# Performance work log

Measured on AMD Instinct MI355X. Metric: run time of the kernel, lower is better.

## Reference

```python
import jax, jax.numpy as jnp
import numpy as np

N = 50000      # nodes
E = 800000     # edges (avg degree 16)
IN, HID, OUT = 128, 256, 64
G = 500        # graphs in the batch (100 nodes each)
NEG_SLOPE = 0.01
EPS = 1e-12


def setup_inputs() -> dict:
    key = jax.random.key(0)
    ks = jax.random.split(key, 9)
    x = jax.random.normal(ks[0], (N, IN), jnp.float32)
    edge_index = jax.random.randint(ks[1], (2, E), 0, N, dtype=jnp.int32)
    # sorted segment ids with every graph present (100 nodes per graph)
    batch = jnp.repeat(jnp.arange(G, dtype=jnp.int32), N // G)
    def lin(k, fan_in, fan_out):
        s = 1.0 / np.sqrt(fan_in)
        kw, kb = jax.random.split(k)
        W = jax.random.uniform(kw, (fan_in, fan_out), jnp.float32, -s, s)
        b = jax.random.uniform(kb, (fan_out,), jnp.float32, -s, s)
        return W, b
    W1, b1 = lin(ks[2], IN, HID)
    W2, b2 = lin(ks[3], HID, HID)
    W3, b3 = lin(ks[4], HID, OUT)
    return {"x": x, "edge_index": edge_index, "batch": batch,
            "W1": W1, "b1": b1, "W2": W2, "b2": b2, "W3": W3, "b3": b3}


def _sage_conv(x, edge_index, W, b):
    # SAGEConv(aggr='add', root_weight=False, normalize=True):
    # gather source features, scatter-add to targets, linear, L2 normalize.
    src, dst = edge_index[0], edge_index[1]
    agg = jax.ops.segment_sum(x[src], dst, num_segments=x.shape[0])  # [N, d_in]
    out = agg @ W + b                                                 # [N, d_out]
    nrm = jnp.linalg.norm(out, axis=-1, keepdims=True)
    return out / jnp.maximum(nrm, EPS)


def reference(x, edge_index, batch, W1, b1, W2, b2, W3, b3):
    h = _sage_conv(x, edge_index, W1, b1)
    h = jax.nn.leaky_relu(h, NEG_SLOPE)          # dropout p=0 -> identity
    h = _sage_conv(h, edge_index, W2, b2)
    h = jax.nn.leaky_relu(h, NEG_SLOPE)
    h = _sage_conv(h, edge_index, W3, b3)
    # get_zero_nodes: first node of each graph (batch sorted, all G present)
    mask = jnp.concatenate([jnp.ones((1,), bool), batch[1:] != batch[:-1]])
    first_idx = jnp.nonzero(mask, size=G)[0]
    return h[first_idx]                          # [G, OUT]
```

## Files before the change

### kernel.cpp

```cpp
#include <hip/hip_runtime.h>

#define N_NODES 50000
#define E_EDGES 800000
#define IN_DIM  128
#define HID_DIM 256
#define OUT_DIM 64
#define G_GRAPHS 500
#define CAP 64
#define NBINS 196
#define BINCAP 5120

typedef __attribute__((ext_vector_type(8))) short short8;
typedef __attribute__((ext_vector_type(4))) float float4v;

__device__ __forceinline__ float bf2f(unsigned short u) {
  union { unsigned int i; float f; } c; c.i = ((unsigned int)u) << 16; return c.f;
}
__device__ __forceinline__ unsigned short f2bf(float f) {
  union { float f; unsigned int i; } c; c.f = f;
  unsigned int x = c.i;
  x += 0x7FFFu + ((x >> 16) & 1u);
  return (unsigned short)(x >> 16);
}
__device__ __forceinline__ unsigned int fbits(float f) {
  union { float f; unsigned int i; } c; c.f = f; return c.i;
}
__device__ __forceinline__ float bits2f(unsigned int u) {
  union { unsigned int i; float f; } c; c.i = u; return c.f;
}


__global__ __launch_bounds__(256) void prep1(
    const int* __restrict__ src, const int* __restrict__ dst,
    const int* __restrict__ batch,
    const float* __restrict__ x,
    const float* __restrict__ W1, const float* __restrict__ W2,
    unsigned int* __restrict__ binbuf, int* __restrict__ bin_next,
    unsigned char* __restrict__ is_first,
    unsigned short* __restrict__ xb,
    unsigned short* __restrict__ W1t, unsigned short* __restrict__ W2t) {
  const int b = blockIdx.x, tid = threadIdx.x;
  if (b < 200) {
    __shared__ int cnt[NBINS];
    __shared__ int gbase[NBINS];
    for (int i = tid; i < NBINS; i += 256) cnt[i] = 0;
    __syncthreads();
    const int base = b * 4096;
    unsigned int pk[16]; int bp[16];
#pragma unroll
    for (int u = 0; u < 16; ++u) {
      const int e = base + u * 256 + tid;
      bp[u] = -1;
      if (e < E_EDGES) {
        const int d = dst[e];
        const int s = src[e];
        const int bin = d >> 8;
        const int pos = atomicAdd(&cnt[bin], 1);
        pk[u] = ((unsigned int)(d & 255) << 16) | (unsigned int)s;
        bp[u] = (bin << 16) | pos;
      }
    }
    __syncthreads();
    for (int i = tid; i < NBINS; i += 256)
      gbase[i] = atomicAdd(&bin_next[i], cnt[i]);
    __syncthreads();
#pragma unroll
    for (int u = 0; u < 16; ++u) {
      if (bp[u] >= 0) {
        const int bin = bp[u] >> 16, pos = bp[u] & 0xFFFF;
        const int idx = gbase[bin] + pos;
        if (idx < BINCAP) binbuf[bin * BINCAP + idx] = pk[u];
      }
    }
  } else if (b < 6450) {
    const int t = (b - 200) * 256 + tid;
    const int i = t * 4;
    const float4 v = *(const float4*)(x + i);
    ushort4 u;
    u.x = f2bf(v.x); u.y = f2bf(v.y); u.z = f2bf(v.z); u.w = f2bf(v.w);
    *(ushort4*)(xb + i) = u;
    if (t < N_NODES) {
      is_first[t] = (t == 0 || batch[t] != batch[t - 1]) ? 1 : 0;
    }
  } else {
    const int t = (b - 6450) * 256 + tid;
    if (t < 8192) {
      const int n = t >> 5, k0 = (t & 31) * 4;
      ushort4 o;
      o.x = f2bf(W1[(k0 + 0) * 256 + n]);
      o.y = f2bf(W1[(k0 + 1) * 256 + n]);
      o.z = f2bf(W1[(k0 + 2) * 256 + n]);
      o.w = f2bf(W1[(k0 + 3) * 256 + n]);
      *(ushort4*)&W1t[n * 128 + k0] = o;
    } else {
      const int v2 = t - 8192;
      const int n = v2 >> 6, k0 = (v2 & 63) * 4;
      ushort4 o;
      o.x = f2bf(W2[(k0 + 0) * 256 + n]);
      o.y = f2bf(W2[(k0 + 1) * 256 + n]);
      o.z = f2bf(W2[(k0 + 2) * 256 + n]);
      o.w = f2bf(W2[(k0 + 3) * 256 + n]);
      *(ushort4*)&W2t[n * 256 + k0] = o;
    }
  }
}


__global__ __launch_bounds__(512) void prep2(
    const unsigned int* __restrict__ binbuf, const int* __restrict__ bin_next,
    const int* __restrict__ batch, const unsigned char* __restrict__ is_first,
    int* __restrict__ deg, unsigned short* __restrict__ srcs,
    unsigned short* __restrict__ list2, int* __restrict__ l2cnt) {
  __shared__ unsigned short img[256 * CAP];
  __shared__ int cnt[256];
  const int tid = threadIdx.x;
  const int bin = blockIdx.x;
  if (tid < 256) cnt[tid] = 0;
  __syncthreads();
  const int total = min(bin_next[bin], BINCAP);
  const unsigned int* bb = binbuf + bin * BINCAP;
  for (int i = tid; i < total; i += 512) {
    const unsigned int pk = bb[i];
    const int nl = pk >> 16;
    const int pos = atomicAdd(&cnt[nl], 1);
    if (pos < CAP) img[(nl << 6) + pos] = (unsigned short)(pk & 0xFFFFu);
  }
  __syncthreads();
  const int node0 = bin << 8;
  const int nend = min(N_NODES, node0 + 256);
  if (tid < 256 && node0 + tid < nend) {
    const int c = cnt[tid];
    deg[node0 + tid] = c;
    if (is_first[node0 + tid]) {
      const int g = batch[node0 + tid];
      l2cnt[g] = min(c, CAP);
      unsigned int* d = (unsigned int*)(list2 + g * 64);
      const unsigned int* s = (const unsigned int*)(img + (tid << 6));
      for (int q = 0; q < 32; ++q) d[q] = s[q];
    }
  }
  const int nwords = (nend - node0) * 32;
  unsigned int* dstw = (unsigned int*)(srcs + ((size_t)node0 << 6));
  const unsigned int* srcw = (const unsigned int*)img;
  for (int i = tid; i < nwords; i += 512) dstw[i] = srcw[i];
}


template<int K, int MODE>
__global__ __launch_bounds__(512, 8) void fused_layer(
    const unsigned short* __restrict__ H,
    const int* __restrict__ deg, const unsigned short* __restrict__ srcs,
    const unsigned short* __restrict__ Wt,
    const float* __restrict__ bias,
    unsigned short* __restrict__ Hout,
    const unsigned short* __restrict__ list2,
    const int* __restrict__ l2cnt,
    float* __restrict__ agg_part)
{
  constexpr int M = 256;
  constexpr int TN = 16;
  constexpr int VPT = K / 64;
  constexpr int LDK = K + 8;
  __shared__ unsigned short a_hi[TN][LDK];
  __shared__ unsigned short a_lo[TN][LDK];
  __shared__ float ssq_tot[TN];
  __shared__ float vld_s[TN];
  __shared__ int nid_s[TN];
  const int tid = threadIdx.x;
  const int lane = tid & 63;
  const int wv = tid >> 6;
  const int graph = blockIdx.x % G_GRAPHS;
  const int p = blockIdx.x / G_GRAPHS;

  if (tid < TN) {
    if constexpr (MODE == 1) {
      const int slot = p * 16 + tid;
      const bool vld = slot < l2cnt[graph];
      nid_s[tid] = vld ? (int)list2[graph * 64 + slot] : 0;
      vld_s[tid] = vld ? 1.f : 0.f;
    } else {
      nid_s[tid] = blockIdx.x * TN + tid;
      vld_s[tid] = 1.f;
    }
    ssq_tot[tid] = 0.f;
  }
  __syncthreads();

  const unsigned short* hb = H + lane * VPT;
  const int node0 = __builtin_amdgcn_readfirstlane(nid_s[2 * wv]);
  const int node1 = __builtin_amdgcn_readfirstlane(nid_s[2 * wv + 1]);
  int cnt0 = __builtin_amdgcn_readfirstlane(min(deg[node0], CAP));
  int cnt1 = __builtin_amdgcn_readfirstlane(min(deg[node1], CAP));
  if constexpr (MODE == 1) {
    if (vld_s[2 * wv] == 0.f) cnt0 = 0;
    if (vld_s[2 * wv + 1] == 0.f) cnt1 = 0;
  }
  int idx0 = 0, idx1 = 0;
  if (lane < cnt0) idx0 = srcs[(node0 << 6) + lane];
  if (lane < cnt1) idx1 = srcs[(node1 << 6) + lane];

  float acc0[VPT], acc1[VPT];
#pragma unroll
  for (int q = 0; q < VPT; ++q) { acc0[q] = 0.f; acc1[q] = 0.f; }
  int j0 = 0, j1 = 0;

  if constexpr (VPT == 2) {
    while (j0 + 16 <= cnt0 && j1 + 16 <= cnt1) {
      int s0[16], s1[16];
#pragma unroll
      for (int u = 0; u < 16; ++u) {
        s0[u] = __builtin_amdgcn_readlane(idx0, j0 + u);
        s1[u] = __builtin_amdgcn_readlane(idx1, j1 + u);
      }
      ushort2 r0[16], r1[16];
#pragma unroll
      for (int u = 0; u < 16; ++u) r0[u] = *(const ushort2*)(hb + s0[u] * K);
#pragma unroll
      for (int u = 0; u < 16; ++u) r1[u] = *(const ushort2*)(hb + s1[u] * K);
#pragma unroll
      for (int u = 0; u < 16; ++u) {
        acc0[0] += bf2f(r0[u].x); acc0[1] += bf2f(r0[u].y);
        acc1[0] += bf2f(r1[u].x); acc1[1] += bf2f(r1[u].y);
      }
      j0 += 16; j1 += 16;
    }
  }

#pragma unroll
  for (int i = 0; i < 2; ++i) {
    const int nn = 2 * wv + i;
    const int cnt = i ? cnt1 : cnt0;
    const int idx = i ? idx1 : idx0;
    float (&acc)[VPT] = i ? acc1 : acc0;
    int j = i ? j1 : j0;

    for (; j + 16 <= cnt; j += 16) {
      int s[16];
#pragma unroll
      for (int u = 0; u < 16; ++u) s[u] = __builtin_amdgcn_readlane(idx, j + u);
      if constexpr (VPT == 4) {
        ushort4 r[16];
#pragma unroll
        for (int u = 0; u < 16; ++u) r[u] = *(const ushort4*)(hb + s[u] * K);
#pragma unroll
        for (int u = 0; u < 16; ++u) {
          acc[0] += bf2f(r[u].x); acc[1] += bf2f(r[u].y);
          acc[2] += bf2f(r[u].z); acc[3] += bf2f(r[u].w);
        }
      } else {
        ushort2 r[16];
#pragma unroll
        for (int u = 0; u < 16; ++u) r[u] = *(const ushort2*)(hb + s[u] * K);
#pragma unroll
        for (int u = 0; u < 16; ++u) {
          acc[0] += bf2f(r[u].x); acc[1] += bf2f(r[u].y);
        }
      }
    }
    for (; j < cnt; j += 8) {
      int s[8]; float w[8];
#pragma unroll
      for (int u = 0; u < 8; ++u) {
        const int q = j + u;
        const int qm = (q < cnt) ? q : (cnt - 1);
        s[u] = __builtin_amdgcn_readlane(idx, qm);
        w[u] = (q < cnt) ? 1.f : 0.f;
      }
      if constexpr (VPT == 4) {
        ushort4 r[8];
#pragma unroll
        for (int u = 0; u < 8; ++u) r[u] = *(const ushort4*)(hb + s[u] * K);
#pragma unroll
        for (int u = 0; u < 8; ++u) {
          acc[0] = fmaf(w[u], bf2f(r[u].x), acc[0]);
          acc[1] = fmaf(w[u], bf2f(r[u].y), acc[1]);
          acc[2] = fmaf(w[u], bf2f(r[u].z), acc[2]);
          acc[3] = fmaf(w[u], bf2f(r[u].w), acc[3]);
        }
      } else {
        ushort2 r[8];
#pragma unroll
        for (int u = 0; u < 8; ++u) r[u] = *(const ushort2*)(hb + s[u] * K);
#pragma unroll
        for (int u = 0; u < 8; ++u) {
          acc[0] = fmaf(w[u], bf2f(r[u].x), acc[0]);
          acc[1] = fmaf(w[u], bf2f(r[u].y), acc[1]);
        }
      }
    }

    unsigned short h[VPT], l[VPT];
#pragma unroll
    for (int jj = 0; jj < VPT; ++jj) {
      const unsigned int u = fbits(acc[jj]);
      h[jj] = (unsigned short)(u >> 16);
      const float res = acc[jj] - bits2f(u & 0xFFFF0000u);
      l[jj] = (unsigned short)(fbits(res) >> 16);
    }
    if constexpr (VPT == 4) {
      *(ushort4*)&a_hi[nn][lane * 4] = make_ushort4(h[0], h[1], h[2], h[3]);
      *(ushort4*)&a_lo[nn][lane * 4] = make_ushort4(l[0], l[1], l[2], l[3]);
    } else {
      *(ushort2*)&a_hi[nn][lane * 2] = make_ushort2(h[0], h[1]);
      *(ushort2*)&a_lo[nn][lane * 2] = make_ushort2(l[0], l[1]);
    }
  }
  __syncthreads();

  const int g = lane >> 4;
  const int lc = lane & 15;
  float4v dacc0 = (float4v){0.f, 0.f, 0.f, 0.f};
  float4v dacc1 = (float4v){0.f, 0.f, 0.f, 0.f};
  const unsigned short* W0 = Wt + (size_t)(wv * 16 + lc) * K + g * 8;
  const unsigned short* W1r = Wt + (size_t)((wv + 8) * 16 + lc) * K + g * 8;
#pragma unroll
  for (int ks = 0; ks < K / 32; ++ks) {
    const short8 ah = *(const short8*)&a_hi[lc][ks * 32 + g * 8];
    const short8 al = *(const short8*)&a_lo[lc][ks * 32 + g * 8];
    const short8 b0 = *(const short8*)(W0 + ks * 32);
    const short8 b1 = *(const short8*)(W1r + ks * 32);
    dacc0 = __builtin_amdgcn_mfma_f32_16x16x32_bf16(ah, b0, dacc0, 0, 0, 0);
    dacc0 = __builtin_amdgcn_mfma_f32_16x16x32_bf16(al, b0, dacc0, 0, 0, 0);
    dacc1 = __builtin_amdgcn_mfma_f32_16x16x32_bf16(ah, b1, dacc1, 0, 0, 0);
    dacc1 = __builtin_amdgcn_mfma_f32_16x16x32_bf16(al, b1, dacc1, 0, 0, 0);
  }

  const float bn0 = bias[wv * 16 + lc];
  const float bn1 = bias[(wv + 8) * 16 + lc];
  float4v o0 = dacc0 + bn0;
  float4v o1 = dacc1 + bn1;
  float sq[4];
#pragma unroll
  for (int r = 0; r < 4; ++r) sq[r] = o0[r] * o0[r] + o1[r] * o1[r];
#pragma unroll
  for (int off = 1; off < 16; off <<= 1) {
#pragma unroll
    for (int r = 0; r < 4; ++r) sq[r] += __shfl_xor(sq[r], off);
  }
  if (lc == 0) {
#pragma unroll
    for (int r = 0; r < 4; ++r) atomicAdd(&ssq_tot[g * 4 + r], sq[r]);
  }
  __syncthreads();

  if constexpr (MODE == 0) {
#pragma unroll
    for (int r = 0; r < 4; ++r) {
      const float inv = 1.f / fmaxf(sqrtf(ssq_tot[g * 4 + r]), 1e-12f);
      float v0 = o0[r] * inv;
      float v1 = o1[r] * inv;
      v0 = (v0 >= 0.f) ? v0 : 0.01f * v0;
      v1 = (v1 >= 0.f) ? v1 : 0.01f * v1;
      const int nd = nid_s[g * 4 + r];
      Hout[(size_t)nd * M + wv * 16 + lc] = f2bf(v0);
      Hout[(size_t)nd * M + (wv + 8) * 16 + lc] = f2bf(v1);
    }
  } else {
    float s0 = 0.f, s1 = 0.f;
#pragma unroll
    for (int r = 0; r < 4; ++r) {
      const float inv = 1.f / fmaxf(sqrtf(ssq_tot[g * 4 + r]), 1e-12f);
      float v0 = o0[r] * inv;
      float v1 = o1[r] * inv;
      v0 = (v0 >= 0.f) ? v0 : 0.01f * v0;
      v1 = (v1 >= 0.f) ? v1 : 0.01f * v1;
      const float w = vld_s[g * 4 + r];
      s0 += w * v0; s1 += w * v1;
    }
    s0 += __shfl_xor(s0, 16); s0 += __shfl_xor(s0, 32);
    s1 += __shfl_xor(s1, 16); s1 += __shfl_xor(s1, 32);
    if (lane < 16) {
      float* pp = agg_part + ((size_t)(graph * 4 + p) << 8);
      pp[wv * 16 + lane] = s0;
      pp[128 + wv * 16 + lane] = s1;
    }
  }
}


__global__ __launch_bounds__(64) void layer3_kernel(
    const float* __restrict__ agg_part,
    const float* __restrict__ W,
    const float* __restrict__ bias,
    float* __restrict__ out)
{
  __shared__ float a_s[HID_DIM];
  const int g = blockIdx.x;
  const int lane = threadIdx.x;
  const float* pp = agg_part + ((size_t)g << 10);
#pragma unroll
  for (int c = 0; c < 4; ++c) {
    const int idx = c * 64 + lane;
    a_s[idx] = pp[idx] + pp[256 + idx] + pp[512 + idx] + pp[768 + idx];
  }
  __syncthreads();
  float o = bias[lane];
#pragma unroll 8
  for (int k = 0; k < HID_DIM; ++k) o += a_s[k] * W[k * OUT_DIM + lane];
  float ss = o * o;
#pragma unroll
  for (int off = 32; off > 0; off >>= 1) ss += __shfl_xor(ss, off);
  const float inv = 1.f / fmaxf(sqrtf(ss), 1e-12f);
  out[(size_t)g * OUT_DIM + lane] = o * inv;
}


extern "C" void kernel_launch(void* const* d_in, const int* in_sizes, int n_in,
                              void* d_out, int out_size, void* d_ws, size_t ws_size,
                              hipStream_t stream) {
  (void)in_sizes; (void)n_in; (void)out_size; (void)ws_size;
  const float* x   = (const float*)d_in[0];
  const int* ei    = (const int*)d_in[1];
  const int* batch = (const int*)d_in[2];
  const float* W1  = (const float*)d_in[3];
  const float* b1  = (const float*)d_in[4];
  const float* W2  = (const float*)d_in[5];
  const float* b2  = (const float*)d_in[6];
  const float* W3  = (const float*)d_in[7];
  const float* b3  = (const float*)d_in[8];
  const int* src = ei;
  const int* dst = ei + E_EDGES;

  char* ws = (char*)d_ws;
  size_t off = 0;
  auto alloc = [&](size_t bytes) {
    void* p = ws + off;
    off = (off + bytes + 255) & ~(size_t)255;
    return p;
  };
  int* bin_next = (int*)alloc((size_t)NBINS * 4);
  const size_t zero_len = off;

  int* deg    = (int*)alloc((size_t)N_NODES * 4);
  unsigned short* srcs = (unsigned short*)alloc((size_t)N_NODES * CAP * 2);
  unsigned char* is_first = (unsigned char*)alloc((size_t)N_NODES);
  unsigned short* list2 = (unsigned short*)alloc((size_t)G_GRAPHS * CAP * 2);
  int* l2cnt  = (int*)alloc((size_t)G_GRAPHS * 4);
  unsigned int* binbuf = (unsigned int*)alloc((size_t)NBINS * BINCAP * 4);
  float* agg_part = (float*)alloc((size_t)G_GRAPHS * 4 * 256 * 4);
  unsigned short* W1t = (unsigned short*)alloc((size_t)256 * 128 * 2);
  unsigned short* W2t = (unsigned short*)alloc((size_t)256 * 256 * 2);
  unsigned short* xb = (unsigned short*)alloc((size_t)N_NODES * IN_DIM * 2);
  unsigned short* h1 = (unsigned short*)alloc((size_t)N_NODES * HID_DIM * 2);

  hipMemsetAsync(bin_next, 0, zero_len, stream);

  prep1<<<6546, 256, 0, stream>>>(src, dst, batch, x, W1, W2,
                                  binbuf, bin_next, is_first, xb, W1t, W2t);
  prep2<<<NBINS, 512, 0, stream>>>(binbuf, bin_next, batch, is_first,
                                   deg, srcs, list2, l2cnt);

  fused_layer<IN_DIM, 0><<<N_NODES / 16, 512, 0, stream>>>(
      xb, deg, srcs, W1t, b1, h1, nullptr, nullptr, nullptr);
  fused_layer<HID_DIM, 1><<<G_GRAPHS * 4, 512, 0, stream>>>(
      h1, deg, srcs, W2t, b2, nullptr, list2, l2cnt, agg_part);
  layer3_kernel<<<G_GRAPHS, 64, 0, stream>>>(agg_part, W3, b3, (float*)d_out);
}
```

Measured before the change: 205.0 us.

## Fuse all stages into one persistent cooperative kernel with grid syncs

Result: slower. 537.1 us (+162.0%).

```diff
diff --git a/kernel.cpp b/kernel.cpp
--- a/kernel.cpp
+++ b/kernel.cpp
@@ -1,4 +1,7 @@
 #include <hip/hip_runtime.h>
+#include <hip/hip_cooperative_groups.h>
+
+namespace cg = cooperative_groups;
 
 #define N_NODES 50000
 #define E_EDGES 800000
@@ -7,8 +10,15 @@
 #define OUT_DIM 64
 #define G_GRAPHS 500
 #define CAP 64
-#define NBINS 196
-#define BINCAP 5120
+#define NBINS 391
+#define BINCAP 2816
+#define NSORT 200
+#define NXCV 3125
+#define NWCV 48
+#define NL1 (N_NODES / 16)
+#define NL2 (G_GRAPHS * 4)
+#define NL3 63
+#define SMEM_BYTES 17536
 
 typedef __attribute__((ext_vector_type(8))) short short8;
 typedef __attribute__((ext_vector_type(4))) float float4v;
@@ -30,92 +40,87 @@
 }
 
 
-__global__ __launch_bounds__(256) void prep1(
+__device__ __forceinline__ void xconv_vb(int v, int tid,
+    const float* __restrict__ x, const int* __restrict__ batch,
+    unsigned char* __restrict__ is_first, unsigned short* __restrict__ xb) {
+  const int t = v * 512 + tid;
+  const int i = t * 4;
+  const float4 vv = *(const float4*)(x + i);
+  ushort4 u;
+  u.x = f2bf(vv.x); u.y = f2bf(vv.y); u.z = f2bf(vv.z); u.w = f2bf(vv.w);
+  *(ushort4*)(xb + i) = u;
+  if (t < N_NODES) is_first[t] = (t == 0 || batch[t] != batch[t - 1]) ? 1 : 0;
+}
+
+__device__ __forceinline__ void wconv_vb(int v, int tid,
+    const float* __restrict__ W1, const float* __restrict__ W2,
+    unsigned short* __restrict__ W1t, unsigned short* __restrict__ W2t) {
+  const int t = v * 512 + tid;
+  if (t < 8192) {
+    const int n = t >> 5, k0 = (t & 31) * 4;
+    ushort4 o;
+    o.x = f2bf(W1[(k0 + 0) * 256 + n]);
+    o.y = f2bf(W1[(k0 + 1) * 256 + n]);
+    o.z = f2bf(W1[(k0 + 2) * 256 + n]);
+    o.w = f2bf(W1[(k0 + 3) * 256 + n]);
+    *(ushort4*)&W1t[n * 128 + k0] = o;
+  } else {
+    const int v2 = t - 8192;
+    const int n = v2 >> 6, k0 = (v2 & 63) * 4;
+    ushort4 o;
+    o.x = f2bf(W2[(k0 + 0) * 256 + n]);
+    o.y = f2bf(W2[(k0 + 1) * 256 + n]);
+    o.z = f2bf(W2[(k0 + 2) * 256 + n]);
+    o.w = f2bf(W2[(k0 + 3) * 256 + n]);
+    *(ushort4*)&W2t[n * 256 + k0] = o;
+  }
+}
+
+__device__ void sort_vb(int sb, int tid, void* smemraw,
     const int* __restrict__ src, const int* __restrict__ dst,
-    const int* __restrict__ batch,
-    const float* __restrict__ x,
-    const float* __restrict__ W1, const float* __restrict__ W2,
-    unsigned int* __restrict__ binbuf, int* __restrict__ bin_next,
-    unsigned char* __restrict__ is_first,
-    unsigned short* __restrict__ xb,
-    unsigned short* __restrict__ W1t, unsigned short* __restrict__ W2t) {
-  const int b = blockIdx.x, tid = threadIdx.x;
-  if (b < 200) {
-    __shared__ int cnt[NBINS];
-    __shared__ int gbase[NBINS];
-    for (int i = tid; i < NBINS; i += 256) cnt[i] = 0;
-    __syncthreads();
-    const int base = b * 4096;
-    unsigned int pk[16]; int bp[16];
-#pragma unroll
-    for (int u = 0; u < 16; ++u) {
-      const int e = base + u * 256 + tid;
-      bp[u] = -1;
-      if (e < E_EDGES) {
-        const int d = dst[e];
-        const int s = src[e];
-        const int bin = d >> 8;
-        const int pos = atomicAdd(&cnt[bin], 1);
-        pk[u] = ((unsigned int)(d & 255) << 16) | (unsigned int)s;
-        bp[u] = (bin << 16) | pos;
-      }
-    }
-    __syncthreads();
-    for (int i = tid; i < NBINS; i += 256)
-      gbase[i] = atomicAdd(&bin_next[i], cnt[i]);
-    __syncthreads();
-#pragma unroll
-    for (int u = 0; u < 16; ++u) {
-      if (bp[u] >= 0) {
-        const int bin = bp[u] >> 16, pos = bp[u] & 0xFFFF;
-        const int idx = gbase[bin] + pos;
-        if (idx < BINCAP) binbuf[bin * BINCAP + idx] = pk[u];
-      }
-    }
-  } else if (b < 6450) {
-    const int t = (b - 200) * 256 + tid;
-    const int i = t * 4;
-    const float4 v = *(const float4*)(x + i);
-    ushort4 u;
-    u.x = f2bf(v.x); u.y = f2bf(v.y); u.z = f2bf(v.z); u.w = f2bf(v.w);
-    *(ushort4*)(xb + i) = u;
-    if (t < N_NODES) {
-      is_first[t] = (t == 0 || batch[t] != batch[t - 1]) ? 1 : 0;
-    }
-  } else {
-    const int t = (b - 6450) * 256 + tid;
-    if (t < 8192) {
-      const int n = t >> 5, k0 = (t & 31) * 4;
-      ushort4 o;
-      o.x = f2bf(W1[(k0 + 0) * 256 + n]);
-      o.y = f2bf(W1[(k0 + 1) * 256 + n]);
-      o.z = f2bf(W1[(k0 + 2) * 256 + n]);
-      o.w = f2bf(W1[(k0 + 3) * 256 + n]);
-      *(ushort4*)&W1t[n * 128 + k0] = o;
-    } else {
-      const int v2 = t - 8192;
-      const int n = v2 >> 6, k0 = (v2 & 63) * 4;
-      ushort4 o;
-      o.x = f2bf(W2[(k0 + 0) * 256 + n]);
-      o.y = f2bf(W2[(k0 + 1) * 256 + n]);
-      o.z = f2bf(W2[(k0 + 2) * 256 + n]);
-      o.w = f2bf(W2[(k0 + 3) * 256 + n]);
-      *(ushort4*)&W2t[n * 256 + k0] = o;
-    }
-  }
-}
-
-
-__global__ __launch_bounds__(512) void prep2(
+    unsigned int* __restrict__ binbuf, int* __restrict__ bin_next) {
+  int* cnt = (int*)smemraw;
+  int* gbase = cnt + NBINS;
+  for (int i = tid; i < NBINS; i += 512) cnt[i] = 0;
+  __syncthreads();
+  const int base = sb * 4096;
+  unsigned int pk[8]; int bp[8];
+#pragma unroll
+  for (int u = 0; u < 8; ++u) {
+    const int e = base + u * 512 + tid;
+    bp[u] = -1;
+    if (e < E_EDGES) {
+      const int d = dst[e];
+      const int s = src[e];
+      const int bin = d >> 7;
+      const int pos = atomicAdd(&cnt[bin], 1);
+      pk[u] = ((unsigned int)(d & 127) << 16) | (unsigned int)s;
+      bp[u] = (bin << 16) | pos;
+    }
+  }
+  __syncthreads();
+  for (int i = tid; i < NBINS; i += 512)
+    gbase[i] = atomicAdd(&bin_next[i], cnt[i]);
+  __syncthreads();
+#pragma unroll
+  for (int u = 0; u < 8; ++u) {
+    if (bp[u] >= 0) {
+      const int bin = bp[u] >> 16, pos = bp[u] & 0xFFFF;
+      const int idx = gbase[bin] + pos;
+      if (idx < BINCAP) binbuf[bin * BINCAP + idx] = pk[u];
+    }
+  }
+  __syncthreads();
+}
+
+__device__ void bucket_vb(int bin, int tid, void* smemraw,
     const unsigned int* __restrict__ binbuf, const int* __restrict__ bin_next,
     const int* __restrict__ batch, const unsigned char* __restrict__ is_first,
     int* __restrict__ deg, unsigned short* __restrict__ srcs,
     unsigned short* __restrict__ list2, int* __restrict__ l2cnt) {
-  __shared__ unsigned short img[256 * CAP];
-  __shared__ int cnt[256];
-  const int tid = threadIdx.x;
-  const int bin = blockIdx.x;
-  if (tid < 256) cnt[tid] = 0;
+  unsigned short* img = (unsigned short*)smemraw;
+  int* cnt = (int*)(img + 128 * CAP);
+  if (tid < 128) cnt[tid] = 0;
   __syncthreads();
   const int total = min(bin_next[bin], BINCAP);
   const unsigned int* bb = binbuf + bin * BINCAP;
@@ -126,51 +131,47 @@
     if (pos < CAP) img[(nl << 6) + pos] = (unsigned short)(pk & 0xFFFFu);
   }
   __syncthreads();
-  const int node0 = bin << 8;
-  const int nend = min(N_NODES, node0 + 256);
-  if (tid < 256 && node0 + tid < nend) {
+  const int node0 = bin << 7;
+  const int nend = min(N_NODES, node0 + 128);
+  if (tid < 128 && node0 + tid < nend) {
     const int c = cnt[tid];
     deg[node0 + tid] = c;
     if (is_first[node0 + tid]) {
       const int g = batch[node0 + tid];
       l2cnt[g] = min(c, CAP);
-      unsigned int* d = (unsigned int*)(list2 + g * 64);
-      const unsigned int* s = (const unsigned int*)(img + (tid << 6));
-      for (int q = 0; q < 32; ++q) d[q] = s[q];
+      unsigned int* dW = (unsigned int*)(list2 + g * 64);
+      const unsigned int* sW = (const unsigned int*)(img + (tid << 6));
+      for (int q = 0; q < 32; ++q) dW[q] = sW[q];
     }
   }
   const int nwords = (nend - node0) * 32;
   unsigned int* dstw = (unsigned int*)(srcs + ((size_t)node0 << 6));
   const unsigned int* srcw = (const unsigned int*)img;
   for (int i = tid; i < nwords; i += 512) dstw[i] = srcw[i];
-}
-
+  __syncthreads();
+}
 
 template<int K, int MODE>
-__global__ __launch_bounds__(512, 8) void fused_layer(
+__device__ void fused_vb(int vb, int tid, void* smemraw,
     const unsigned short* __restrict__ H,
     const int* __restrict__ deg, const unsigned short* __restrict__ srcs,
-    const unsigned short* __restrict__ Wt,
-    const float* __restrict__ bias,
+    const unsigned short* __restrict__ Wt, const float* __restrict__ bias,
     unsigned short* __restrict__ Hout,
-    const unsigned short* __restrict__ list2,
-    const int* __restrict__ l2cnt,
-    float* __restrict__ agg_part)
-{
+    const unsigned short* __restrict__ list2, const int* __restrict__ l2cnt,
+    float* __restrict__ agg_part) {
   constexpr int M = 256;
   constexpr int TN = 16;
   constexpr int VPT = K / 64;
   constexpr int LDK = K + 8;
-  __shared__ unsigned short a_hi[TN][LDK];
-  __shared__ unsigned short a_lo[TN][LDK];
-  __shared__ float ssq_tot[TN];
-  __shared__ float vld_s[TN];
-  __shared__ int nid_s[TN];
-  const int tid = threadIdx.x;
+  unsigned short (*a_hi)[LDK] = (unsigned short(*)[LDK])smemraw;
+  unsigned short (*a_lo)[LDK] = (unsigned short(*)[LDK])((char*)smemraw + TN * LDK * 2);
+  float* ssq_tot = (float*)((char*)smemraw + TN * LDK * 4);
+  float* vld_s = ssq_tot + TN;
+  int* nid_s = (int*)(vld_s + TN);
   const int lane = tid & 63;
   const int wv = tid >> 6;
-  const int graph = blockIdx.x % G_GRAPHS;
-  const int p = blockIdx.x / G_GRAPHS;
+  const int graph = vb % G_GRAPHS;
+  const int p = vb / G_GRAPHS;
 
   if (tid < TN) {
     if constexpr (MODE == 1) {
@@ -179,7 +180,7 @@
       nid_s[tid] = vld ? (int)list2[graph * 64 + slot] : 0;
       vld_s[tid] = vld ? 1.f : 0.f;
     } else {
-      nid_s[tid] = blockIdx.x * TN + tid;
+      nid_s[tid] = vb * TN + tid;
       vld_s[tid] = 1.f;
     }
     ssq_tot[tid] = 0.f;
@@ -375,33 +376,100 @@
       pp[128 + wv * 16 + lane] = s1;
     }
   }
-}
-
-
-__global__ __launch_bounds__(64) void layer3_kernel(
-    const float* __restrict__ agg_part,
-    const float* __restrict__ W,
-    const float* __restrict__ bias,
-    float* __restrict__ out)
-{
-  __shared__ float a_s[HID_DIM];
-  const int g = blockIdx.x;
-  const int lane = threadIdx.x;
-  const float* pp = agg_part + ((size_t)g << 10);
-#pragma unroll
-  for (int c = 0; c < 4; ++c) {
-    const int idx = c * 64 + lane;
-    a_s[idx] = pp[idx] + pp[256 + idx] + pp[512 + idx] + pp[768 + idx];
-  }
-  __syncthreads();
-  float o = bias[lane];
+  __syncthreads();
+}
+
+__device__ void l3_vb(int v, int tid, void* smemraw,
+    const float* __restrict__ agg_part, const float* __restrict__ W,
+    const float* __restrict__ bias, float* __restrict__ out) {
+  const int wv = tid >> 6, lane = tid & 63;
+  const int g = v * 8 + wv;
+  float* a_s = (float*)smemraw + wv * 256;
+  if (g < G_GRAPHS) {
+    const float* pp = agg_part + ((size_t)g << 10);
+#pragma unroll
+    for (int c = 0; c < 4; ++c) {
+      const int idx = c * 64 + lane;
+      a_s[idx] = pp[idx] + pp[256 + idx] + pp[512 + idx] + pp[768 + idx];
+    }
+  }
+  __syncthreads();
+  if (g < G_GRAPHS) {
+    float o = bias[lane];
 #pragma unroll 8
-  for (int k = 0; k < HID_DIM; ++k) o += a_s[k] * W[k * OUT_DIM + lane];
-  float ss = o * o;
-#pragma unroll
-  for (int off = 32; off > 0; off >>= 1) ss += __shfl_xor(ss, off);
-  const float inv = 1.f / fmaxf(sqrtf(ss), 1e-12f);
-  out[(size_t)g * OUT_DIM + lane] = o * inv;
+    for (int k = 0; k < HID_DIM; ++k) o += a_s[k] * W[k * OUT_DIM + lane];
+    float ss = o * o;
+#pragma unroll
+    for (int off = 32; off > 0; off >>= 1) ss += __shfl_xor(ss, off);
+    const float inv = 1.f / fmaxf(sqrtf(ss), 1e-12f);
+    out[(size_t)g * OUT_DIM + lane] = o * inv;
+  }
+  __syncthreads();
+}
+
+__global__ __launch_bounds__(512, 8) void mega(
+    const int* src, const int* dst, const int* batch, const float* x,
+    const float* W1, const float* W2, const float* b1, const float* b2,
+    const float* W3, const float* b3,
+    unsigned int* binbuf, int* bin_next, unsigned char* is_first,
+    unsigned short* xb, unsigned short* W1t, unsigned short* W2t,
+    int* deg, unsigned short* srcs, unsigned short* list2, int* l2cnt,
+    unsigned short* h1, float* agg_part, float* outp) {
+  __shared__ __align__(16) char smem[SMEM_BYTES];
+  cg::grid_group grid = cg::this_grid();
+  const int tid = threadIdx.x;
+  const int nb = gridDim.x;
+  for (int v = blockIdx.x; v < NXCV + NWCV + NSORT; v += nb) {
+    if (v < NXCV) xconv_vb(v, tid, x, batch, is_first, xb);
+    else if (v < NXCV + NWCV) wconv_vb(v - NXCV, tid, W1, W2, W1t, W2t);
+    else sort_vb(v - NXCV - NWCV, tid, smem, src, dst, binbuf, bin_next);
+  }
+  grid.sync();
+  for (int v = blockIdx.x; v < NBINS; v += nb)
+    bucket_vb(v, tid, smem, binbuf, bin_next, batch, is_first, deg, srcs, list2, l2cnt);
+  grid.sync();
+  for (int v = blockIdx.x; v < NL1; v += nb)
+    fused_vb<IN_DIM, 0>(v, tid, smem, xb, deg, srcs, W1t, b1, h1, nullptr, nullptr, nullptr);
+  grid.sync();
+  for (int v = blockIdx.x; v < NL2; v += nb)
+    fused_vb<HID_DIM, 1>(v, tid, smem, h1, deg, srcs, W2t, b2, nullptr, list2, l2cnt, agg_part);
+  grid.sync();
+  for (int v = blockIdx.x; v < NL3; v += nb)
+    l3_vb(v, tid, smem, agg_part, W3, b3, outp);
+}
+
+__global__ __launch_bounds__(512, 8) void wrapA1(
+    const int* src, const int* dst, const int* batch, const float* x,
+    const float* W1, const float* W2,
+    unsigned int* binbuf, int* bin_next, unsigned char* is_first,
+    unsigned short* xb, unsigned short* W1t, unsigned short* W2t) {
+  __shared__ __align__(16) char smem[SMEM_BYTES];
+  const int v = blockIdx.x, tid = threadIdx.x;
+  if (v < NXCV) xconv_vb(v, tid, x, batch, is_first, xb);
+  else if (v < NXCV + NWCV) wconv_vb(v - NXCV, tid, W1, W2, W1t, W2t);
+  else sort_vb(v - NXCV - NWCV, tid, smem, src, dst, binbuf, bin_next);
+}
+__global__ __launch_bounds__(512, 8) void wrapA2(
+    const unsigned int* binbuf, const int* bin_next, const int* batch,
+    const unsigned char* is_first, int* deg, unsigned short* srcs,
+    unsigned short* list2, int* l2cnt) {
+  __shared__ __align__(16) char smem[SMEM_BYTES];
+  bucket_vb(blockIdx.x, threadIdx.x, smem, binbuf, bin_next, batch, is_first,
+            deg, srcs, list2, l2cnt);
+}
+template<int K, int MODE>
+__global__ __launch_bounds__(512, 8) void wrapF(
+    const unsigned short* H, const int* deg, const unsigned short* srcs,
+    const unsigned short* Wt, const float* bias, unsigned short* Hout,
+    const unsigned short* list2, const int* l2cnt, float* agg_part) {
+  __shared__ __align__(16) char smem[SMEM_BYTES];
+  fused_vb<K, MODE>(blockIdx.x, threadIdx.x, smem, H, deg, srcs, Wt, bias,
+                    Hout, list2, l2cnt, agg_part);
+}
+__global__ __launch_bounds__(512, 8) void wrapD(
+    const float* agg_part, const float* W, const float* bias, float* out) {
+  __shared__ __align__(16) char smem[SMEM_BYTES];
+  l3_vb(blockIdx.x, threadIdx.x, smem, agg_part, W, bias, out);
 }
 
 
@@ -420,6 +488,7 @@
   const float* b3  = (const float*)d_in[8];
   const int* src = ei;
   const int* dst = ei + E_EDGES;
+  float* outp = (float*)d_out;
 
   char* ws = (char*)d_ws;
   size_t off = 0;
@@ -430,7 +499,6 @@
   };
   int* bin_next = (int*)alloc((size_t)NBINS * 4);
   const size_t zero_len = off;
-
   int* deg    = (int*)alloc((size_t)N_NODES * 4);
   unsigned short* srcs = (unsigned short*)alloc((size_t)N_NODES * CAP * 2);
   unsigned char* is_first = (unsigned char*)alloc((size_t)N_NODES);
@@ -445,14 +513,32 @@
 
   hipMemsetAsync(bin_next, 0, zero_len, stream);
 
-  prep1<<<6546, 256, 0, stream>>>(src, dst, batch, x, W1, W2,
-                                  binbuf, bin_next, is_first, xb, W1t, W2t);
-  prep2<<<NBINS, 512, 0, stream>>>(binbuf, bin_next, batch, is_first,
-                                   deg, srcs, list2, l2cnt);
-
-  fused_layer<IN_DIM, 0><<<N_NODES / 16, 512, 0, stream>>>(
-      xb, deg, srcs, W1t, b1, h1, nullptr, nullptr, nullptr);
-  fused_layer<HID_DIM, 1><<<G_GRAPHS * 4, 512, 0, stream>>>(
-      h1, deg, srcs, W2t, b2, nullptr, list2, l2cnt, agg_part);
-  layer3_kernel<<<G_GRAPHS, 64, 0, stream>>>(agg_part, W3, b3, (float*)d_out);
-}
+  int occ = 0;
+  hipOccupancyMaxActiveBlocksPerMultiprocessor(&occ, mega, 512, 0);
+  int grid = occ * 256;
+  if (grid > 1024) grid = 1024;
+  bool coop = (grid >= 256);
+  if (coop) {
+    void* args[] = {
+      (void*)&src, (void*)&dst, (void*)&batch, (void*)&x,
+      (void*)&W1, (void*)&W2, (void*)&b1, (void*)&b2, (void*)&W3, (void*)&b3,
+      (void*)&binbuf, (void*)&bin_next, (void*)&is_first,
+      (void*)&xb, (void*)&W1t, (void*)&W2t,
+      (void*)&deg, (void*)&srcs, (void*)&list2, (void*)&l2cnt,
+      (void*)&h1, (void*)&agg_part, (void*)&outp };
+    hipError_t e = hipLaunchCooperativeKernel(mega, dim3(grid), dim3(512),
+                                              args, 0u, stream);
+    coop = (e == hipSuccess);
+  }
+  if (!coop) {
+    wrapA1<<<NXCV + NWCV + NSORT, 512, 0, stream>>>(
+        src, dst, batch, x, W1, W2, binbuf, bin_next, is_first, xb, W1t, W2t);
+    wrapA2<<<NBINS, 512, 0, stream>>>(
+        binbuf, bin_next, batch, is_first, deg, srcs, list2, l2cnt);
+    wrapF<IN_DIM, 0><<<NL1, 512, 0, stream>>>(
+        xb, deg, srcs, W1t, b1, h1, nullptr, nullptr, nullptr);
+    wrapF<HID_DIM, 1><<<NL2, 512, 0, stream>>>(
+        h1, deg, srcs, W2t, b2, nullptr, list2, l2cnt, agg_part);
+    wrapD<<<NL3, 512, 0, stream>>>(agg_part, W3, b3, outp);
+  }
+}
```

## Split wave into half-waves per node with wider gathers; skip empty layer-2 blocks

Applied to the files above, without the earlier changes.

New measurement: 201.6 us. Within noise of the previous version (-1.7%).

```diff
diff --git a/kernel.cpp b/kernel.cpp
--- a/kernel.cpp
+++ b/kernel.cpp
@@ -12,6 +12,8 @@
 
 typedef __attribute__((ext_vector_type(8))) short short8;
 typedef __attribute__((ext_vector_type(4))) float float4v;
+typedef __attribute__((ext_vector_type(4))) unsigned short u16x4;
+typedef __attribute__((ext_vector_type(8))) unsigned short u16x8;
 
 __device__ __forceinline__ float bf2f(unsigned short u) {
   union { unsigned int i; float f; } c; c.i = ((unsigned int)u) << 16; return c.f;
@@ -159,7 +161,8 @@
 {
   constexpr int M = 256;
   constexpr int TN = 16;
-  constexpr int VPT = K / 64;
+  constexpr int CH = K / 32;
+  constexpr int DEPTH = (CH == 4) ? 16 : 8;
   constexpr int LDK = K + 8;
   __shared__ unsigned short a_hi[TN][LDK];
   __shared__ unsigned short a_lo[TN][LDK];
@@ -172,6 +175,10 @@
   const int graph = blockIdx.x % G_GRAPHS;
   const int p = blockIdx.x / G_GRAPHS;
 
+  if constexpr (MODE == 1) {
+    if (p * 16 >= l2cnt[graph]) return;
+  }
+
   if (tid < TN) {
     if constexpr (MODE == 1) {
       const int slot = p * 16 + tid;
@@ -186,7 +193,8 @@
   }
   __syncthreads();
 
-  const unsigned short* hb = H + lane * VPT;
+  const int half = lane >> 5;
+  const int li = lane & 31;
   const int node0 = __builtin_amdgcn_readfirstlane(nid_s[2 * wv]);
   const int node1 = __builtin_amdgcn_readfirstlane(nid_s[2 * wv + 1]);
   int cnt0 = __builtin_amdgcn_readfirstlane(min(deg[node0], CAP));
@@ -198,111 +206,75 @@
   int idx0 = 0, idx1 = 0;
   if (lane < cnt0) idx0 = srcs[(node0 << 6) + lane];
   if (lane < cnt1) idx1 = srcs[(node1 << 6) + lane];
-
-  float acc0[VPT], acc1[VPT];
-#pragma unroll
-  for (int q = 0; q < VPT; ++q) { acc0[q] = 0.f; acc1[q] = 0.f; }
-  int j0 = 0, j1 = 0;
-
-  if constexpr (VPT == 2) {
-    while (j0 + 16 <= cnt0 && j1 + 16 <= cnt1) {
-      int s0[16], s1[16];
-#pragma unroll
-      for (int u = 0; u < 16; ++u) {
-        s0[u] = __builtin_amdgcn_readlane(idx0, j0 + u);
-        s1[u] = __builtin_amdgcn_readlane(idx1, j1 + u);
-      }
-      ushort2 r0[16], r1[16];
-#pragma unroll
-      for (int u = 0; u < 16; ++u) r0[u] = *(const ushort2*)(hb + s0[u] * K);
-#pragma unroll
-      for (int u = 0; u < 16; ++u) r1[u] = *(const ushort2*)(hb + s1[u] * K);
-#pragma unroll
-      for (int u = 0; u < 16; ++u) {
-        acc0[0] += bf2f(r0[u].x); acc0[1] += bf2f(r0[u].y);
-        acc1[0] += bf2f(r1[u].x); acc1[1] += bf2f(r1[u].y);
-      }
-      j0 += 16; j1 += 16;
-    }
-  }
-
-#pragma unroll
-  for (int i = 0; i < 2; ++i) {
-    const int nn = 2 * wv + i;
-    const int cnt = i ? cnt1 : cnt0;
-    const int idx = i ? idx1 : idx0;
-    float (&acc)[VPT] = i ? acc1 : acc0;
-    int j = i ? j1 : j0;
-
-    for (; j + 16 <= cnt; j += 16) {
-      int s[16];
-#pragma unroll
-      for (int u = 0; u < 16; ++u) s[u] = __builtin_amdgcn_readlane(idx, j + u);
-      if constexpr (VPT == 4) {
-        ushort4 r[16];
-#pragma unroll
-        for (int u = 0; u < 16; ++u) r[u] = *(const ushort4*)(hb + s[u] * K);
-#pragma unroll
-        for (int u = 0; u < 16; ++u) {
-          acc[0] += bf2f(r[u].x); acc[1] += bf2f(r[u].y);
-          acc[2] += bf2f(r[u].z); acc[3] += bf2f(r[u].w);
-        }
-      } else {
-        ushort2 r[16];
-#pragma unroll
-        for (int u = 0; u < 16; ++u) r[u] = *(const ushort2*)(hb + s[u] * K);
-#pragma unroll
-        for (int u = 0; u < 16; ++u) {
-          acc[0] += bf2f(r[u].x); acc[1] += bf2f(r[u].y);
-        }
-      }
-    }
-    for (; j < cnt; j += 8) {
-      int s[8]; float w[8];
-#pragma unroll
-      for (int u = 0; u < 8; ++u) {
-        const int q = j + u;
-        const int qm = (q < cnt) ? q : (cnt - 1);
-        s[u] = __builtin_amdgcn_readlane(idx, qm);
-        w[u] = (q < cnt) ? 1.f : 0.f;
-      }
-      if constexpr (VPT == 4) {
-        ushort4 r[8];
-#pragma unroll
-        for (int u = 0; u < 8; ++u) r[u] = *(const ushort4*)(hb + s[u] * K);
-#pragma unroll
-        for (int u = 0; u < 8; ++u) {
-          acc[0] = fmaf(w[u], bf2f(r[u].x), acc[0]);
-          acc[1] = fmaf(w[u], bf2f(r[u].y), acc[1]);
-          acc[2] = fmaf(w[u], bf2f(r[u].z), acc[2]);
-          acc[3] = fmaf(w[u], bf2f(r[u].w), acc[3]);
-        }
-      } else {
-        ushort2 r[8];
-#pragma unroll
-        for (int u = 0; u < 8; ++u) r[u] = *(const ushort2*)(hb + s[u] * K);
-#pragma unroll
-        for (int u = 0; u < 8; ++u) {
-          acc[0] = fmaf(w[u], bf2f(r[u].x), acc[0]);
-          acc[1] = fmaf(w[u], bf2f(r[u].y), acc[1]);
-        }
-      }
-    }
-
-    unsigned short h[VPT], l[VPT];
-#pragma unroll
-    for (int jj = 0; jj < VPT; ++jj) {
-      const unsigned int u = fbits(acc[jj]);
-      h[jj] = (unsigned short)(u >> 16);
-      const float res = acc[jj] - bits2f(u & 0xFFFF0000u);
-      l[jj] = (unsigned short)(fbits(res) >> 16);
-    }
-    if constexpr (VPT == 4) {
-      *(ushort4*)&a_hi[nn][lane * 4] = make_ushort4(h[0], h[1], h[2], h[3]);
-      *(ushort4*)&a_lo[nn][lane * 4] = make_ushort4(l[0], l[1], l[2], l[3]);
+  const int cmy = half ? cnt1 : cnt0;
+  const unsigned short* hb2 = H + li * CH;
+
+  float acc[CH];
+#pragma unroll
+  for (int ch = 0; ch < CH; ++ch) acc[ch] = 0.f;
+  const int cmax = max(cnt0, cnt1);
+
+  for (int j = 0; j < cmax; j += DEPTH) {
+    int sa[DEPTH], sb[DEPTH];
+#pragma unroll
+    for (int u = 0; u < DEPTH; ++u) {
+      const int q = j + u;
+      const int q0 = (cnt0 > 0) ? ((q < cnt0) ? q : cnt0 - 1) : 0;
+      const int q1 = (cnt1 > 0) ? ((q < cnt1) ? q : cnt1 - 1) : 0;
+      sa[u] = __builtin_amdgcn_readlane(idx0, q0);
+      sb[u] = __builtin_amdgcn_readlane(idx1, q1);
+    }
+    if constexpr (CH == 4) {
+      u16x4 r[DEPTH];
+#pragma unroll
+      for (int u = 0; u < DEPTH; ++u) {
+        const int s = half ? sb[u] : sa[u];
+        r[u] = *(const u16x4*)(hb2 + s * K);
+      }
+#pragma unroll
+      for (int u = 0; u < DEPTH; ++u) {
+        const float w = (j + u < cmy) ? 1.f : 0.f;
+#pragma unroll
+        for (int ch = 0; ch < 4; ++ch) acc[ch] = fmaf(w, bf2f(r[u][ch]), acc[ch]);
+      }
     } else {
-      *(ushort2*)&a_hi[nn][lane * 2] = make_ushort2(h[0], h[1]);
-      *(ushort2*)&a_lo[nn][lane * 2] = make_ushort2(l[0], l[1]);
+      u16x8 r[DEPTH];
+#pragma unroll
+      for (int u = 0; u < DEPTH; ++u) {
+        const int s = half ? sb[u] : sa[u];
+        r[u] = *(const u16x8*)(hb2 + s * K);
+      }
+#pragma unroll
+      for (int u = 0; u < DEPTH; ++u) {
+        const float w = (j + u < cmy) ? 1.f : 0.f;
+#pragma unroll
+        for (int ch = 0; ch < 8; ++ch) acc[ch] = fmaf(w, bf2f(r[u][ch]), acc[ch]);
+      }
+    }
+  }
+
+  {
+    unsigned short hs[CH], ls[CH];
+#pragma unroll
+    for (int ch = 0; ch < CH; ++ch) {
+      const unsigned int u = fbits(acc[ch]);
+      hs[ch] = (unsigned short)(u >> 16);
+      const float res = acc[ch] - bits2f(u & 0xFFFF0000u);
+      ls[ch] = (unsigned short)(fbits(res) >> 16);
+    }
+    const int nn = 2 * wv + half;
+    if constexpr (CH == 4) {
+      u16x4 hv, lv;
+#pragma unroll
+      for (int ch = 0; ch < 4; ++ch) { hv[ch] = hs[ch]; lv[ch] = ls[ch]; }
+      *(u16x4*)&a_hi[nn][li * 4] = hv;
+      *(u16x4*)&a_lo[nn][li * 4] = lv;
+    } else {
+      u16x8 hv, lv;
+#pragma unroll
+      for (int ch = 0; ch < 8; ++ch) { hv[ch] = hs[ch]; lv[ch] = ls[ch]; }
+      *(u16x8*)&a_hi[nn][li * 8] = hv;
+      *(u16x8*)&a_lo[nn][li * 8] = lv;
     }
   }
   __syncthreads();
@@ -380,6 +352,7 @@
 
 __global__ __launch_bounds__(64) void layer3_kernel(
     const float* __restrict__ agg_part,
+    const int* __restrict__ l2cnt,
     const float* __restrict__ W,
     const float* __restrict__ bias,
     float* __restrict__ out)
@@ -387,11 +360,14 @@
   __shared__ float a_s[HID_DIM];
   const int g = blockIdx.x;
   const int lane = threadIdx.x;
+  const int nq = (min(l2cnt[g], CAP) + 15) >> 4;
   const float* pp = agg_part + ((size_t)g << 10);
 #pragma unroll
   for (int c = 0; c < 4; ++c) {
     const int idx = c * 64 + lane;
-    a_s[idx] = pp[idx] + pp[256 + idx] + pp[512 + idx] + pp[768 + idx];
+    float s = 0.f;
+    for (int q = 0; q < nq; ++q) s += pp[q * 256 + idx];
+    a_s[idx] = s;
   }
   __syncthreads();
   float o = bias[lane];
@@ -454,5 +430,5 @@
       xb, deg, srcs, W1t, b1, h1, nullptr, nullptr, nullptr);
   fused_layer<HID_DIM, 1><<<G_GRAPHS * 4, 512, 0, stream>>>(
       h1, deg, srcs, W2t, b2, nullptr, list2, l2cnt, agg_part);
-  layer3_kernel<<<G_GRAPHS, 64, 0, stream>>>(agg_part, W3, b3, (float*)d_out);
-}
+  layer3_kernel<<<G_GRAPHS, 64, 0, stream>>>(agg_part, l2cnt, W3, b3, (float*)d_out);
+}
```
